# Optimization experiments

Hardware: AMD Instinct MI355X
Metric: run time of the kernel (lower is better)

## Reference

```python
import jax, jax.numpy as jnp
import numpy as np

CHANNEL = 256
REDUCTION = 16
HIDDEN = CHANNEL // REDUCTION          # 16
BILINEAR_DIM = HIDDEN * HIDDEN         # 256


def setup_inputs() -> dict:
    key = jax.random.key(0)
    k_x, k_w1, k_w2 = jax.random.split(key, 3)
    x = jax.random.normal(k_x, (32, CHANNEL, 64, 64), dtype=jnp.float32)
    # torch nn.Linear(in, out, bias=False) stores weight as [out, in]
    w1 = jax.random.normal(k_w1, (HIDDEN, CHANNEL), dtype=jnp.float32) * (1.0 / np.sqrt(CHANNEL))
    w2 = jax.random.normal(k_w2, (CHANNEL, BILINEAR_DIM), dtype=jnp.float32) * (1.0 / np.sqrt(BILINEAR_DIM))
    return {"x": x, "w1": w1, "w2": w2}


def reference(x, w1, w2):
    b, c, h, w = x.shape
    # global average pool -> [b, c]
    pooled = jnp.mean(x, axis=(2, 3))
    # fc1 + ReLU -> [b, hidden]
    y = jax.nn.relu(jnp.einsum('bc,hc->bh', pooled, w1))
    # batched outer product -> [b, hidden, hidden], flattened to [b, hidden^2]
    outer = (y[:, :, None] * y[:, None, :]).reshape(b, -1)
    # fc2 + sigmoid -> [b, c]
    s = jax.nn.sigmoid(jnp.einsum('bd,cd->bc', outer, w2))
    # channel-wise scale
    return x * s[:, :, None, None]
```

## Files before the change

### kernel.cpp

```cpp
#include <hip/hip_runtime.h>
#include <math.h>


#define B 32
#define C 256
#define HID 16
#define BD 256
#define HW 4096

typedef float vf4 __attribute__((ext_vector_type(4)));

__global__ __launch_bounds__(256) void pool_kernel(const float* __restrict__ x,
                                                   float* __restrict__ pooled) {
    const int bc = blockIdx.x;
    const vf4* xp = reinterpret_cast<const vf4*>(x + (size_t)bc * HW);
    const int t = threadIdx.x;
    float sum = 0.f;
#pragma unroll
    for (int k = 0; k < 4; ++k) {
        vf4 v = xp[t + k * 256];
        sum += (v.x + v.y) + (v.z + v.w);
    }
#pragma unroll
    for (int off = 32; off > 0; off >>= 1) sum += __shfl_down(sum, off, 64);
    __shared__ float ws[4];
    const int lane = t & 63, wid = t >> 6;
    if (lane == 0) ws[wid] = sum;
    __syncthreads();
    if (t == 0) {
        float tot = (ws[0] + ws[1]) + (ws[2] + ws[3]);
        pooled[bc] = tot * (1.0f / (float)HW);
    }
}

__global__ __launch_bounds__(256) void fc_kernel(const float* __restrict__ pooled,
                                                 const float* __restrict__ w1,
                                                 const float* __restrict__ w2,
                                                 float* __restrict__ s_out) {
    const int b = blockIdx.x;
    const int t = threadIdx.x;
    __shared__ float pl[C];
    __shared__ float yv[HID];
    __shared__ float outer[BD];

    pl[t] = pooled[b * C + t];
    __syncthreads();

    if (t < HID) {
        float acc = 0.f;
        const float* w1r = w1 + t * C;
#pragma unroll 8
        for (int c = 0; c < C; ++c) acc += pl[c] * w1r[c];
        yv[t] = fmaxf(acc, 0.f);
    }
    __syncthreads();

    outer[t] = yv[t >> 4] * yv[t & 15];
    __syncthreads();

    const vf4* w2r = reinterpret_cast<const vf4*>(w2 + (size_t)t * BD);
    const vf4* orow = reinterpret_cast<const vf4*>(outer);
    float acc = 0.f;
#pragma unroll 8
    for (int d4 = 0; d4 < BD / 4; ++d4) {
        vf4 w = w2r[d4];
        vf4 o = orow[d4];
        acc += w.x * o.x + w.y * o.y + w.z * o.z + w.w * o.w;
    }
    s_out[b * C + t] = 1.0f / (1.0f + expf(-acc));
}

__global__ __launch_bounds__(256) void scale_kernel(const float* __restrict__ x,
                                                    const float* __restrict__ s,
                                                    float* __restrict__ out) {
    const int bc = blockIdx.x;
    const float sc = s[bc];
    const vf4* xp = reinterpret_cast<const vf4*>(x + (size_t)bc * HW);
    vf4* op = reinterpret_cast<vf4*>(out + (size_t)bc * HW);
    const int t = threadIdx.x;
#pragma unroll
    for (int k = 0; k < 4; ++k) {
        vf4 v = xp[t + k * 256];
        v *= sc;
        __builtin_nontemporal_store(v, &op[t + k * 256]);
    }
}

extern "C" void kernel_launch(void* const* d_in, const int* in_sizes, int n_in,
                              void* d_out, int out_size, void* d_ws, size_t ws_size,
                              hipStream_t stream) {
    const float* x  = (const float*)d_in[0];
    const float* w1 = (const float*)d_in[1];
    const float* w2 = (const float*)d_in[2];
    float* out = (float*)d_out;

    float* pooled = (float*)d_ws;
    float* s      = (float*)d_ws + B * C;

    pool_kernel<<<B * C, 256, 0, stream>>>(x, pooled);
    fc_kernel<<<B, 256, 0, stream>>>(pooled, w1, w2, s);
    scale_kernel<<<B * C, 256, 0, stream>>>(x, s, out);
}
```

Baseline: 77.47 us.

## Fuse FC into scale kernel and chunk batches for L2 reuse

Removes the separate fc kernel. Each scale block now recomputes fc1 for its batch and a single fc2 dot product for its channel, then scales its x tile. The batch is also processed in two chunks of 16, so the x data read by pooling may still be in cache (MI355X has a large last-level cache) when the scale pass reads it again. The cost is redundant fc1 work in every block and four launches instead of three.

```diff
diff --git a/kernel.cpp b/kernel.cpp
--- a/kernel.cpp
+++ b/kernel.cpp
@@ -7,12 +7,14 @@
 #define HID 16
 #define BD 256
 #define HW 4096
+#define CHUNKB 16
 
 typedef float vf4 __attribute__((ext_vector_type(4)));
 
 __global__ __launch_bounds__(256) void pool_kernel(const float* __restrict__ x,
-                                                   float* __restrict__ pooled) {
-    const int bc = blockIdx.x;
+                                                   float* __restrict__ pooled,
+                                                   int bc0) {
+    const int bc = bc0 + blockIdx.x;
     const vf4* xp = reinterpret_cast<const vf4*>(x + (size_t)bc * HW);
     const int t = threadIdx.x;
     float sum = 0.f;
@@ -23,67 +25,68 @@
     }
 #pragma unroll
     for (int off = 32; off > 0; off >>= 1) sum += __shfl_down(sum, off, 64);
-    __shared__ float ws[4];
-    const int lane = t & 63, wid = t >> 6;
-    if (lane == 0) ws[wid] = sum;
+    __shared__ float red[4];
+    if ((t & 63) == 0) red[t >> 6] = sum;
     __syncthreads();
-    if (t == 0) {
-        float tot = (ws[0] + ws[1]) + (ws[2] + ws[3]);
-        pooled[bc] = tot * (1.0f / (float)HW);
-    }
+    if (t == 0)
+        pooled[bc] = ((red[0] + red[1]) + (red[2] + red[3])) * (1.0f / (float)HW);
 }
 
-__global__ __launch_bounds__(256) void fc_kernel(const float* __restrict__ pooled,
-                                                 const float* __restrict__ w1,
-                                                 const float* __restrict__ w2,
-                                                 float* __restrict__ s_out) {
-    const int b = blockIdx.x;
+__global__ __launch_bounds__(256) void scale_kernel(const float* __restrict__ x,
+                                                    const float* __restrict__ pooled,
+                                                    const float* __restrict__ w1,
+                                                    const float* __restrict__ w2,
+                                                    float* __restrict__ out,
+                                                    int bc0) {
+    const int bc = bc0 + blockIdx.x;
+    const int b = bc >> 8, c0 = bc & 255;
     const int t = threadIdx.x;
+
+    const vf4* xp = reinterpret_cast<const vf4*>(x + (size_t)bc * HW);
+    vf4 v0 = xp[t];
+    vf4 v1 = xp[t + 256];
+    vf4 v2 = xp[t + 512];
+    vf4 v3 = xp[t + 768];
+
     __shared__ float pl[C];
     __shared__ float yv[HID];
-    __shared__ float outer[BD];
+    __shared__ float red[4];
+    __shared__ float sc_sh;
 
     pl[t] = pooled[b * C + t];
     __syncthreads();
 
-    if (t < HID) {
-        float acc = 0.f;
-        const float* w1r = w1 + t * C;
-#pragma unroll 8
-        for (int c = 0; c < C; ++c) acc += pl[c] * w1r[c];
-        yv[t] = fmaxf(acc, 0.f);
+    {
+        const int h = t >> 4, j = t & 15;
+        const float* w1r = w1 + h * C + j * 16;
+        const float* plr = pl + j * 16;
+        float p = 0.f;
+#pragma unroll
+        for (int k = 0; k < 16; ++k) p += plr[k] * w1r[k];
+        p += __shfl_xor(p, 1, 64);
+        p += __shfl_xor(p, 2, 64);
+        p += __shfl_xor(p, 4, 64);
+        p += __shfl_xor(p, 8, 64);
+        if (j == 0) yv[h] = fmaxf(p, 0.f);
     }
     __syncthreads();
 
-    outer[t] = yv[t >> 4] * yv[t & 15];
+    float term = yv[t >> 4] * yv[t & 15] * w2[(size_t)c0 * BD + t];
+#pragma unroll
+    for (int off = 32; off > 0; off >>= 1) term += __shfl_down(term, off, 64);
+    if ((t & 63) == 0) red[t >> 6] = term;
     __syncthreads();
+    if (t == 0)
+        sc_sh = 1.0f / (1.0f + expf(-((red[0] + red[1]) + (red[2] + red[3]))));
+    __syncthreads();
+    const float sc = sc_sh;
 
-    const vf4* w2r = reinterpret_cast<const vf4*>(w2 + (size_t)t * BD);
-    const vf4* orow = reinterpret_cast<const vf4*>(outer);
-    float acc = 0.f;
-#pragma unroll 8
-    for (int d4 = 0; d4 < BD / 4; ++d4) {
-        vf4 w = w2r[d4];
-        vf4 o = orow[d4];
-        acc += w.x * o.x + w.y * o.y + w.z * o.z + w.w * o.w;
-    }
-    s_out[b * C + t] = 1.0f / (1.0f + expf(-acc));
-}
-
-__global__ __launch_bounds__(256) void scale_kernel(const float* __restrict__ x,
-                                                    const float* __restrict__ s,
-                                                    float* __restrict__ out) {
-    const int bc = blockIdx.x;
-    const float sc = s[bc];
-    const vf4* xp = reinterpret_cast<const vf4*>(x + (size_t)bc * HW);
     vf4* op = reinterpret_cast<vf4*>(out + (size_t)bc * HW);
-    const int t = threadIdx.x;
-#pragma unroll
-    for (int k = 0; k < 4; ++k) {
-        vf4 v = xp[t + k * 256];
-        v *= sc;
-        __builtin_nontemporal_store(v, &op[t + k * 256]);
-    }
+    v0 *= sc; v1 *= sc; v2 *= sc; v3 *= sc;
+    __builtin_nontemporal_store(v0, &op[t]);
+    __builtin_nontemporal_store(v1, &op[t + 256]);
+    __builtin_nontemporal_store(v2, &op[t + 512]);
+    __builtin_nontemporal_store(v3, &op[t + 768]);
 }
 
 extern "C" void kernel_launch(void* const* d_in, const int* in_sizes, int n_in,
@@ -95,9 +98,10 @@
     float* out = (float*)d_out;
 
     float* pooled = (float*)d_ws;
-    float* s      = (float*)d_ws + B * C;
 
-    pool_kernel<<<B * C, 256, 0, stream>>>(x, pooled);
-    fc_kernel<<<B, 256, 0, stream>>>(pooled, w1, w2, s);
-    scale_kernel<<<B * C, 256, 0, stream>>>(x, s, out);
+    for (int cb = 0; cb < B; cb += CHUNKB) {
+        const int bc0 = cb * C;
+        pool_kernel<<<CHUNKB * C, 256, 0, stream>>>(x, pooled, bc0);
+        scale_kernel<<<CHUNKB * C, 256, 0, stream>>>(x, pooled, w1, w2, out, bc0);
+    }
 }
```

After: 67.58 us. 12.8% less time.
